# Performance work log

Measured on AMD Instinct MI355X. Metric: run time of the kernel, lower is better.

The kernel has to match this reference:

```python
import jax, jax.numpy as jnp
import numpy as np

MODES_KEPT = 64  # n_modes=(128,) -> 128//2 rfft modes retained (neuralop convention)
N_LAYERS = 4     # neuralop FNO default n_layers
PAD_FRAC = 0.1   # domain_padding


def setup_inputs() -> dict:
    key = jax.random.key(0)
    ks = jax.random.split(key, 24)
    B, T, P = 128, 4096, 64
    E, Hemb, W = 32, 128, 64
    Cin = 4 + E            # 36
    Hl = 2 * W             # lifting hidden (lifting_channel_ratio=2)
    Hp = 2 * W             # projection hidden

    def w(k, sh):
        fan_in = sh[0]
        return jax.random.normal(k, sh, jnp.float32) * (fan_in ** -0.5)

    spec_scale = 1.0 / (W * W)
    return {
        "v_terminals": jax.random.normal(ks[0], (B, 4, T), jnp.float32),
        "physical_params": jax.random.normal(ks[1], (B, P), jnp.float32),
        # DeviceEmbedding MLP: P -> Hemb -> Hemb -> E
        "emb_w1": w(ks[2], (P, Hemb)), "emb_b1": jnp.zeros((Hemb,), jnp.float32),
        "emb_w2": w(ks[3], (Hemb, Hemb)), "emb_b2": jnp.zeros((Hemb,), jnp.float32),
        "emb_w3": w(ks[4], (Hemb, E)), "emb_b3": jnp.zeros((E,), jnp.float32),
        # FNO lifting channel-MLP: Cin -> Hl -> W (pointwise over time)
        "lift_w1": w(ks[5], (Cin, Hl)), "lift_b1": jnp.zeros((Hl,), jnp.float32),
        "lift_w2": w(ks[6], (Hl, W)), "lift_b2": jnp.zeros((W,), jnp.float32),
        # spectral conv complex weights, stored as real/imag: (L, Cin=W, Cout=W, M)
        "spec_wr": jax.random.normal(ks[7], (N_LAYERS, W, W, MODES_KEPT), jnp.float32) * spec_scale,
        "spec_wi": jax.random.normal(ks[8], (N_LAYERS, W, W, MODES_KEPT), jnp.float32) * spec_scale,
        # linear (1x1) skips per layer
        "skip_w": jax.random.normal(ks[9], (N_LAYERS, W, W), jnp.float32) * (W ** -0.5),
        "skip_b": jnp.zeros((N_LAYERS, W), jnp.float32),
        # projection channel-MLP: W -> Hp -> 1
        "proj_w1": w(ks[10], (W, Hp)), "proj_b1": jnp.zeros((Hp,), jnp.float32),
        "proj_w2": w(ks[11], (Hp, 1)), "proj_b2": jnp.zeros((1,), jnp.float32),
    }


def _chan_mlp(x, w, b):
    # pointwise channel linear on (B, C, T)
    return jnp.einsum("bct,cd->bdt", x, w) + b[None, :, None]


def reference(v_terminals, physical_params,
              emb_w1, emb_b1, emb_w2, emb_b2, emb_w3, emb_b3,
              lift_w1, lift_b1, lift_w2, lift_b2,
              spec_wr, spec_wi, skip_w, skip_b,
              proj_w1, proj_b1, proj_w2, proj_b2):
    silu = jax.nn.silu
    gelu = jax.nn.gelu
    B, _, T = v_terminals.shape
    # device embedding: Linear-GELU-Linear-GELU-Linear-Tanh
    h = gelu(physical_params @ emb_w1 + emb_b1)
    h = gelu(h @ emb_w2 + emb_b2)
    h = jnp.tanh(h @ emb_w3 + emb_b3)                       # (B, E)
    lat = jnp.broadcast_to(h[:, :, None], (B, h.shape[1], T))
    x = jnp.concatenate([v_terminals, lat], axis=1)          # (B, 36, T)
    # lifting
    x = _chan_mlp(silu(_chan_mlp(x, lift_w1, lift_b1) * 0 + _chan_mlp(x, lift_w1, lift_b1)), lift_w2, lift_b2) if False else None
    x = jnp.concatenate([v_terminals, lat], axis=1)
    x = _chan_mlp(x, lift_w1, lift_b1)
    x = silu(x)
    x = _chan_mlp(x, lift_w2, lift_b2)                       # (B, W, T)
    pad = int(round(PAD_FRAC * T))
    x = jnp.pad(x, ((0, 0), (0, 0), (0, pad)))
    Tp = T + pad
    nfreq = Tp // 2 + 1
    for l in range(N_LAYERS):
        hpre = silu(x)                                       # preactivation
        skip = jnp.einsum("bct,oc->bot", hpre, skip_w[l]) + skip_b[l][None, :, None]
        xf = jnp.fft.rfft(hpre, axis=-1)                     # (B, W, nfreq) complex
        wc = spec_wr[l] + 1j * spec_wi[l]                    # (W, W, M)
        yf = jnp.einsum("bcm,com->bom", xf[..., :MODES_KEPT], wc)
        out_ft = jnp.pad(yf, ((0, 0), (0, 0), (0, nfreq - MODES_KEPT)))
        x = jnp.fft.irfft(out_ft, n=Tp, axis=-1) + skip
    x = x[..., :T]                                           # unpad
    # projection
    x = _chan_mlp(x, proj_w1, proj_b1)
    x = silu(x)
    x = _chan_mlp(x, proj_w2, proj_b2)                       # (B, 1, T)
    return x
```

## Files before the change

kernel.cpp:

```cpp
#include <hip/hip_runtime.h>
#include <math.h>

#define B_     128
#define T_     4096
#define TP_    4506
#define TPAD_  4608
#define KSPLIT 6
#define NL_    4

typedef __attribute__((ext_vector_type(8))) short bf16x8;
typedef __attribute__((ext_vector_type(4))) float f32x4;
typedef unsigned short u16;

__device__ __forceinline__ float silu_f(float x){
  return x / (1.0f + expf(-x));
}
__device__ __forceinline__ float gelu_f(float x){
  float u = x + 0.044715f*x*x*x;
  return 0.5f*x*(1.0f + tanhf(0.7978845608028654f*u));
}
__device__ __forceinline__ u16 bf16_rne(float f){
  unsigned u = __float_as_uint(f);
  unsigned r = u + 0x7FFFu + ((u >> 16) & 1u);
  return (u16)(r >> 16);
}
__device__ __forceinline__ void bf16_split(float f, u16& h, u16& l){
  h = bf16_rne(f);
  float fh = __uint_as_float(((unsigned)h) << 16);
  l = bf16_rne(f - fh);
}
__device__ __forceinline__ void silu_split(float v, u16& h, u16& l){
  float s = v / (1.0f + __expf(-v));
  bf16_split(s, h, l);
}
__device__ __forceinline__ f32x4 mfma16(bf16x8 a, bf16x8 b, f32x4 c){
  return __builtin_amdgcn_mfma_f32_16x16x32_bf16(a, b, c, 0, 0, 0);
}

#define FMA8x8(ACC, A0, A1, B0, B1) do {                                   \
  float av_[8] = {A0.x,A0.y,A0.z,A0.w,A1.x,A1.y,A1.z,A1.w};                \
  float bv_[8] = {B0.x,B0.y,B0.z,B0.w,B1.x,B1.y,B1.z,B1.w};                \
  _Pragma("unroll")                                                        \
  for(int i_=0;i_<8;i_++){                                                 \
    _Pragma("unroll")                                                      \
    for(int j_=0;j_<8;j_++) ACC[i_][j_] += av_[i_]*bv_[j_];                \
  }                                                                        \
} while(0)

__global__ __launch_bounds__(256) void k_tables(u16* __restrict__ fwdFh,
    u16* __restrict__ fwdFl, u16* __restrict__ invFh, u16* __restrict__ invFl){
  int idx = blockIdx.x*256 + threadIdx.x;
  if(idx >= TPAD_*64) return;
  int t = idx >> 6, m = idx & 63;
  float c = 0.f, s = 0.f;
  if(t < TP_){
    int r = (int)(((long long)m * (long long)t) % TP_);
    double ang = 6.283185307179586476925287 * (double)r / (double)TP_;
    c = (float)cos(ang);
    s = -(float)sin(ang);
  }
  u16 ch, cl, sh, sl;
  bf16_split(c, ch, cl);
  bf16_split(s, sh, sl);
  fwdFh[t*128 + m] = ch;      fwdFl[t*128 + m] = cl;
  fwdFh[t*128 + 64 + m] = sh; fwdFl[t*128 + 64 + m] = sl;
  invFh[(long)m*TPAD_ + t] = ch;      invFl[(long)m*TPAD_ + t] = cl;
  invFh[(long)(64+m)*TPAD_ + t] = sh; invFl[(long)(64+m)*TPAD_ + t] = sl;
}

__global__ __launch_bounds__(256) void k_prep(const float* __restrict__ skw,
    u16* __restrict__ skwh, u16* __restrict__ skwl){
  int i = blockIdx.x*256 + threadIdx.x;
  if(i >= NL_*64*64) return;
  u16 h, l; bf16_split(skw[i], h, l);
  skwh[i] = h; skwl[i] = l;
}

__global__ __launch_bounds__(128) void k_embed(
    const float* __restrict__ pp,
    const float* __restrict__ ew1, const float* __restrict__ eb1,
    const float* __restrict__ ew2, const float* __restrict__ eb2,
    const float* __restrict__ ew3, const float* __restrict__ eb3,
    const float* __restrict__ lw1, const float* __restrict__ lb1,
    float* __restrict__ latb)
{
  int b = blockIdx.x, tid = threadIdx.x;
  __shared__ float p[64], h1[128], h2[128], e[32];
  if(tid < 64) p[tid] = pp[b*64 + tid];
  __syncthreads();
  {
    float z = eb1[tid];
    for(int j=0;j<64;j++) z += p[j]*ew1[j*128 + tid];
    h1[tid] = gelu_f(z);
  }
  __syncthreads();
  {
    float z = eb2[tid];
    for(int j=0;j<128;j++) z += h1[j]*ew2[j*128 + tid];
    h2[tid] = gelu_f(z);
  }
  __syncthreads();
  if(tid < 32){
    float z = eb3[tid];
    for(int j=0;j<128;j++) z += h2[j]*ew3[j*32 + tid];
    e[tid] = tanhf(z);
  }
  __syncthreads();
  {
    float v = lb1[tid];
    for(int c=0;c<32;c++) v += e[c]*lw1[(4+c)*128 + tid];
    latb[b*128 + tid] = v;
  }
}

__global__ __launch_bounds__(128) void k_lift(
    const float* __restrict__ vterm, const float* __restrict__ latb,
    const float* __restrict__ lw1,  const float* __restrict__ lw2,
    const float* __restrict__ lb2,  float* __restrict__ x)
{
  int tt = blockIdx.x, b = blockIdx.y, tid = threadIdx.x;
  int t0 = tt*128;
  if(t0 >= T_){
    int r = tid >> 1, tcb = (tid & 1)*64;
    float4 z4 = make_float4(0.f,0.f,0.f,0.f);
    #pragma unroll
    for(int q=0;q<16;q++)
      *(float4*)(x + ((long)b*64 + r)*TPAD_ + t0 + tcb + q*4) = z4;
    return;
  }
  __shared__ float w2s[128*64];
  __shared__ float zt[64*132];
  __shared__ float vt[4*128];
  #pragma unroll
  for(int q=0;q<16;q++){
    int idx = q*512 + tid*4;
    *(float4*)(w2s + idx) = *(const float4*)(lw2 + idx);
  }
  {
    int c = tid >> 5, tc = (tid & 31)*4;
    *(float4*)(vt + c*128 + tc) =
      *(const float4*)(vterm + ((long)b*4 + c)*T_ + t0 + tc);
  }
  int tx = tid & 15, ty = tid >> 4;
  float acc[8][8];
  #pragma unroll
  for(int i=0;i<8;i++){
    #pragma unroll
    for(int j=0;j<8;j++) acc[i][j] = 0.f;
  }
  for(int ch=0; ch<2; ++ch){
    __syncthreads();
    {
      int dl = tid >> 1, d = ch*64 + dl, tcb = (tid & 1)*64;
      float lb  = latb[b*128 + d];
      float wc0 = lw1[0*128 + d], wc1 = lw1[1*128 + d];
      float wc2 = lw1[2*128 + d], wc3 = lw1[3*128 + d];
      #pragma unroll
      for(int q=0;q<16;q++){
        int tc = tcb + q*4;
        float4 v0 = *(const float4*)(vt + 0*128 + tc);
        float4 v1 = *(const float4*)(vt + 1*128 + tc);
        float4 v2 = *(const float4*)(vt + 2*128 + tc);
        float4 v3 = *(const float4*)(vt + 3*128 + tc);
        float4 z;
        z.x = silu_f(lb + wc0*v0.x + wc1*v1.x + wc2*v2.x + wc3*v3.x);
        z.y = silu_f(lb + wc0*v0.y + wc1*v1.y + wc2*v2.y + wc3*v3.y);
        z.z = silu_f(lb + wc0*v0.z + wc1*v1.z + wc2*v2.z + wc3*v3.z);
        z.w = silu_f(lb + wc0*v0.w + wc1*v1.w + wc2*v2.w + wc3*v3.w);
        *(float4*)(zt + dl*132 + tc) = z;
      }
    }
    __syncthreads();
    #pragma unroll 4
    for(int k=0;k<64;k++){
      int d = ch*64 + k;
      float4 a0 = *(const float4*)(w2s + d*64 + 8*ty);
      float4 a1 = *(const float4*)(w2s + d*64 + 8*ty + 4);
      float4 b0 = *(const float4*)(zt + k*132 + 8*tx);
      float4 b1 = *(const float4*)(zt + k*132 + 8*tx + 4);
      FMA8x8(acc, a0, a1, b0, b1);
    }
  }
  #pragma unroll
  for(int i=0;i<8;i++){
    int w = 8*ty + i;
    float bias = lb2[w];
    float* dst = x + ((long)b*64 + w)*TPAD_ + t0 + 8*tx;
    *(float4*)(dst)   = make_float4(acc[i][0]+bias, acc[i][1]+bias, acc[i][2]+bias, acc[i][3]+bias);
    *(float4*)(dst+4) = make_float4(acc[i][4]+bias, acc[i][5]+bias, acc[i][6]+bias, acc[i][7]+bias);
  }
}

__global__ __launch_bounds__(256) void k_dft_mfma(
    const float* __restrict__ x, const u16* __restrict__ invFh,
    const u16* __restrict__ invFl, float* __restrict__ xfp)
{
  int b = blockIdx.x, s = blockIdx.y;
  int tid = threadIdx.x;
  int lane = tid & 63, w = tid >> 6;
  int l15 = lane & 15, lhi = lane >> 4;
  int n0 = w*32;
  __shared__ u16 ah[64*128];
  __shared__ u16 al[64*128];
  f32x4 acc[4][2];
  #pragma unroll
  for(int mi=0;mi<4;mi++){
    #pragma unroll
    for(int ni=0;ni<2;ni++) acc[mi][ni] = (f32x4){0.f,0.f,0.f,0.f};
  }
  for(int ch=0; ch<6; ++ch){
    int k0 = s*768 + ch*128;
    __syncthreads();
    {
      int c = tid >> 2;
      const float* xr = x + ((long)b*64 + c)*TPAD_ + k0;
      int swz = (c & 7) << 4;
      #pragma unroll
      for(int q=0;q<8;q++){
        int tl = ((tid & 3) + 4*q)*4;
        float4 v = *(const float4*)(xr + tl);
        ushort4 hv, lv;
        silu_split(v.x, hv.x, lv.x);
        silu_split(v.y, hv.y, lv.y);
        silu_split(v.z, hv.z, lv.z);
        silu_split(v.w, hv.w, lv.w);
        int byt = (c*256 + tl*2) ^ swz;
        *(ushort4*)((char*)ah + byt) = hv;
        *(ushort4*)((char*)al + byt) = lv;
      }
    }
    __syncthreads();
    #pragma unroll
    for(int ks=0; ks<4; ++ks){
      bf16x8 Ah[4], Al[4], Bh[2], Bl[2];
      #pragma unroll
      for(int mi=0;mi<4;mi++){
        int c = mi*16 + l15;
        int byt = (c*256 + (ks*32 + lhi*8)*2) ^ ((c & 7) << 4);
        Ah[mi] = *(bf16x8*)((char*)ah + byt);
        Al[mi] = *(bf16x8*)((char*)al + byt);
      }
      #pragma unroll
      for(int ni=0;ni<2;ni++){
        int j = n0 + ni*16 + l15;
        long off = (long)j*TPAD_ + k0 + ks*32 + lhi*8;
        Bh[ni] = *(const bf16x8*)(invFh + off);
        Bl[ni] = *(const bf16x8*)(invFl + off);
      }
      #pragma unroll
      for(int mi=0;mi<4;mi++){
        #pragma unroll
        for(int ni=0;ni<2;ni++){
          acc[mi][ni] = mfma16(Ah[mi], Bh[ni], acc[mi][ni]);
          acc[mi][ni] = mfma16(Al[mi], Bh[ni], acc[mi][ni]);
          acc[mi][ni] = mfma16(Ah[mi], Bl[ni], acc[mi][ni]);
        }
      }
    }
  }
  #pragma unroll
  for(int mi=0;mi<4;mi++){
    #pragma unroll
    for(int ni=0;ni<2;ni++){
      #pragma unroll
      for(int r=0;r<4;r++){
        int row = mi*16 + lhi*4 + r;
        int j = n0 + ni*16 + l15;
        xfp[((long)s*8192 + b*64 + row)*128 + j] = acc[mi][ni][r];
      }
    }
  }
}

__global__ __launch_bounds__(512) void k_spectral(
    const float* __restrict__ xfp, const float* __restrict__ wr_,
    const float* __restrict__ wi_, u16* __restrict__ coefh,
    u16* __restrict__ coefl, int l)
{
  int b = blockIdx.x, mh = blockIdx.y, tid = threadIdx.x;
  const float* wr = wr_ + (long)l*262144;
  const float* wi = wi_ + (long)l*262144;
  __shared__ float xr[64*36], xi[64*36];
  {
    int c = tid >> 3, mm0 = (tid & 7)*4;
    long base = ((long)(b*64 + c))*128 + mh*32 + mm0;
    float4 sr = make_float4(0.f,0.f,0.f,0.f), si = sr;
    #pragma unroll
    for(int s2=0;s2<KSPLIT;s2++){
      const float* p = xfp + (long)s2*1048576 + base;
      float4 a = *(const float4*)(p);
      float4 d = *(const float4*)(p + 64);
      sr.x += a.x; sr.y += a.y; sr.z += a.z; sr.w += a.w;
      si.x += d.x; si.y += d.y; si.z += d.z; si.w += d.w;
    }
    *(float4*)(xr + c*36 + mm0) = sr;
    *(float4*)(xi + c*36 + mm0) = si;
  }
  __syncthreads();
  int tx = tid & 15, ty = tid >> 4;
  float ar[2][2] = {{0.f,0.f},{0.f,0.f}};
  float ai[2][2] = {{0.f,0.f},{0.f,0.f}};
  #pragma unroll 2
  for(int c=0;c<64;c++){
    float x0r = xr[c*36 + 2*tx], x1r = xr[c*36 + 2*tx + 1];
    float x0i = xi[c*36 + 2*tx], x1i = xi[c*36 + 2*tx + 1];
    #pragma unroll
    for(int oi=0;oi<2;oi++){
      int o = 2*ty + oi;
      long wofs = ((long)(c*64 + o))*64 + mh*32 + 2*tx;
      float2 wrv = *(const float2*)(wr + wofs);
      float2 wiv = *(const float2*)(wi + wofs);
      ar[oi][0] += x0r*wrv.x - x0i*wiv.x;
      ai[oi][0] += x0r*wiv.x + x0i*wrv.x;
      ar[oi][1] += x1r*wrv.y - x1i*wiv.y;
      ai[oi][1] += x1r*wiv.y + x1i*wrv.y;
    }
  }
  #pragma unroll
  for(int j=0;j<2;j++){
    int m = mh*32 + 2*tx + j;
    float sc = (m==0) ? (1.0f/(float)TP_) : (2.0f/(float)TP_);
    #pragma unroll
    for(int oi=0;oi<2;oi++){
      int o = 2*ty + oi;
      long base = ((long)b*64 + o)*128;
      u16 h, l2;
      bf16_split(sc*ar[oi][j], h, l2);
      coefh[base + m] = h; coefl[base + m] = l2;
      bf16_split(sc*ai[oi][j], h, l2);
      coefh[base + 64 + m] = h; coefl[base + 64 + m] = l2;
    }
  }
}

__global__ __launch_bounds__(256) void k_idft_mfma(
    float* __restrict__ x, const u16* __restrict__ coefh,
    const u16* __restrict__ coefl, const u16* __restrict__ fwdFh,
    const u16* __restrict__ fwdFl, const u16* __restrict__ skwh,
    const u16* __restrict__ skwl, const float* __restrict__ sb_, int lay)
{
  int tt = blockIdx.x, b = blockIdx.y, tid = threadIdx.x;
  int t0 = tt*128;
  int lane = tid & 63, w = tid >> 6;
  int l15 = lane & 15, lhi = lane >> 4;
  int n0 = w*32;
  __shared__ u16 hh[128*64];
  __shared__ u16 hl[128*64];
  {
    int cp = tid & 31, tg = tid >> 3 >> 2;
    int c0 = cp*2;
    const float* xr0 = x + ((long)b*64 + c0)*TPAD_ + t0 + tg*16;
    const float* xr1 = xr0 + TPAD_;
    #pragma unroll
    for(int q=0;q<4;q++){
      float4 v0 = *(const float4*)(xr0 + q*4);
      float4 v1 = *(const float4*)(xr1 + q*4);
      float e0[4] = {v0.x, v0.y, v0.z, v0.w};
      float e1[4] = {v1.x, v1.y, v1.z, v1.w};
      #pragma unroll
      for(int i=0;i<4;i++){
        int t = tg*16 + q*4 + i;
        u16 h0, l0, h1, l1;
        silu_split(e0[i], h0, l0);
        silu_split(e1[i], h1, l1);
        int byt = (t*128 + c0*2) ^ ((t & 7) << 4);
        *(ushort2*)((char*)hh + byt) = make_ushort2(h0, h1);
        *(ushort2*)((char*)hl + byt) = make_ushort2(l0, l1);
      }
    }
  }
  f32x4 acc[4][2];
  #pragma unroll
  for(int mi=0;mi<4;mi++){
    #pragma unroll
    for(int ni=0;ni<2;ni++) acc[mi][ni] = (f32x4){0.f,0.f,0.f,0.f};
  }
  #pragma unroll
  for(int ks=0; ks<4; ++ks){
    bf16x8 Ah[4], Al[4], Bh[2], Bl[2];
    #pragma unroll
    for(int mi=0;mi<4;mi++){
      int o = mi*16 + l15;
      long off = ((long)(b*64 + o))*128 + ks*32 + lhi*8;
      Ah[mi] = *(const bf16x8*)(coefh + off);
      Al[mi] = *(const bf16x8*)(coefl + off);
    }
    #pragma unroll
    for(int ni=0;ni<2;ni++){
      int t = t0 + n0 + ni*16 + l15;
      long off = (long)t*128 + ks*32 + lhi*8;
      Bh[ni] = *(const bf16x8*)(fwdFh + off);
      Bl[ni] = *(const bf16x8*)(fwdFl + off);
    }
    #pragma unroll
    for(int mi=0;mi<4;mi++){
      #pragma unroll
      for(int ni=0;ni<2;ni++){
        acc[mi][ni] = mfma16(Ah[mi], Bh[ni], acc[mi][ni]);
        acc[mi][ni] = mfma16(Al[mi], Bh[ni], acc[mi][ni]);
        acc[mi][ni] = mfma16(Ah[mi], Bl[ni], acc[mi][ni]);
      }
    }
  }
  __syncthreads();
  #pragma unroll
  for(int ks=0; ks<2; ++ks){
    bf16x8 Ah[4], Al[4], Bh[2], Bl[2];
    #pragma unroll
    for(int mi=0;mi<4;mi++){
      int o = mi*16 + l15;
      long off = (long)lay*4096 + o*64 + ks*32 + lhi*8;
      Ah[mi] = *(const bf16x8*)(skwh + off);
      Al[mi] = *(const bf16x8*)(skwl + off);
    }
    #pragma unroll
    for(int ni=0;ni<2;ni++){
      int t = n0 + ni*16 + l15;
      int byt = (t*128 + (ks*32 + lhi*8)*2) ^ ((t & 7) << 4);
      Bh[ni] = *(bf16x8*)((char*)hh + byt);
      Bl[ni] = *(bf16x8*)((char*)hl + byt);
    }
    #pragma unroll
    for(int mi=0;mi<4;mi++){
      #pragma unroll
      for(int ni=0;ni<2;ni++){
        acc[mi][ni] = mfma16(Ah[mi], Bh[ni], acc[mi][ni]);
        acc[mi][ni] = mfma16(Al[mi], Bh[ni], acc[mi][ni]);
        acc[mi][ni] = mfma16(Ah[mi], Bl[ni], acc[mi][ni]);
      }
    }
  }
  #pragma unroll
  for(int mi=0;mi<4;mi++){
    #pragma unroll
    for(int ni=0;ni<2;ni++){
      #pragma unroll
      for(int r=0;r<4;r++){
        int o = mi*16 + lhi*4 + r;
        int t = t0 + n0 + ni*16 + l15;
        float v = acc[mi][ni][r] + sb_[lay*64 + o];
        if(t >= TP_) v = 0.f;
        x[((long)b*64 + o)*TPAD_ + t] = v;
      }
    }
  }
}

__global__ __launch_bounds__(256) void k_proj(
    const float* __restrict__ x,  const float* __restrict__ pw1,
    const float* __restrict__ pb1, const float* __restrict__ pw2,
    const float* __restrict__ pb2, float* __restrict__ out)
{
  int tt = blockIdx.x, b = blockIdx.y, tid = threadIdx.x;
  int t0 = tt*128;
  __shared__ float w1s[64*128];
  __shared__ float xt[64*132];
  __shared__ float red[16*132];
  #pragma unroll
  for(int q=0;q<8;q++){
    int idx = q*1024 + tid*4;
    *(float4*)(w1s + idx) = *(const float4*)(pw1 + idx);
  }
  {
    int w = tid >> 2, tc0 = (tid & 3)*4;
    #pragma unroll
    for(int q=0;q<8;q++){
      int tc = tc0 + q*16;
      *(float4*)(xt + w*132 + tc) =
        *(const float4*)(x + ((long)b*64 + w)*TPAD_ + t0 + tc);
    }
  }
  __syncthreads();
  int tx = tid & 15, ty = tid >> 4;
  float acc[8][8];
  #pragma unroll
  for(int i=0;i<8;i++){
    #pragma unroll
    for(int j=0;j<8;j++) acc[i][j] = 0.f;
  }
  #pragma unroll 4
  for(int k=0;k<64;k++){
    float4 a0 = *(const float4*)(w1s + k*128 + 8*ty);
    float4 a1 = *(const float4*)(w1s + k*128 + 8*ty + 4);
    float4 b0 = *(const float4*)(xt + k*132 + 8*tx);
    float4 b1 = *(const float4*)(xt + k*132 + 8*tx + 4);
    FMA8x8(acc, a0, a1, b0, b1);
  }
  float part[8];
  #pragma unroll
  for(int j=0;j<8;j++) part[j] = 0.f;
  #pragma unroll
  for(int i=0;i<8;i++){
    int d = 8*ty + i;
    float bb = pb1[d], w2v = pw2[d];
    #pragma unroll
    for(int j=0;j<8;j++) part[j] += w2v * silu_f(acc[i][j] + bb);
  }
  *(float4*)(red + ty*132 + 8*tx)     = make_float4(part[0],part[1],part[2],part[3]);
  *(float4*)(red + ty*132 + 8*tx + 4) = make_float4(part[4],part[5],part[6],part[7]);
  __syncthreads();
  if(tid < 128){
    float ssum = pb2[0];
    #pragma unroll
    for(int y=0;y<16;y++) ssum += red[y*132 + tid];
    out[(long)b*T_ + t0 + tid] = ssum;
  }
}

extern "C" void kernel_launch(void* const* d_in, const int* in_sizes, int n_in,
                              void* d_out, int out_size, void* d_ws, size_t ws_size,
                              hipStream_t stream)
{
  const float* vterm = (const float*)d_in[0];
  const float* pp    = (const float*)d_in[1];
  const float* ew1   = (const float*)d_in[2];
  const float* eb1   = (const float*)d_in[3];
  const float* ew2   = (const float*)d_in[4];
  const float* eb2   = (const float*)d_in[5];
  const float* ew3   = (const float*)d_in[6];
  const float* eb3   = (const float*)d_in[7];
  const float* lw1   = (const float*)d_in[8];
  const float* lb1   = (const float*)d_in[9];
  const float* lw2   = (const float*)d_in[10];
  const float* lb2   = (const float*)d_in[11];
  const float* swr   = (const float*)d_in[12];
  const float* swi   = (const float*)d_in[13];
  const float* skw   = (const float*)d_in[14];
  const float* skb   = (const float*)d_in[15];
  const float* pw1   = (const float*)d_in[16];
  const float* pb1   = (const float*)d_in[17];
  const float* pw2   = (const float*)d_in[18];
  const float* pb2   = (const float*)d_in[19];
  float* out = (float*)d_out;
  float* ws  = (float*)d_ws;

  float* x    = ws;
  float* xfp  = x + (long)B_*64*TPAD_;
  u16* coefh  = (u16*)(xfp + (long)KSPLIT*8192*128);
  u16* coefl  = coefh + 1048576;
  u16* fwdFh  = coefl + 1048576;
  u16* fwdFl  = fwdFh + 589824;
  u16* invFh  = fwdFl + 589824;
  u16* invFl  = invFh + 589824;
  u16* skwh   = invFl + 589824;
  u16* skwl   = skwh + 16384;
  float* latb = (float*)coefh;

  k_tables<<<(TPAD_*64 + 255)/256, 256, 0, stream>>>(fwdFh, fwdFl, invFh, invFl);
  k_prep<<<(NL_*64*64 + 255)/256, 256, 0, stream>>>(skw, skwh, skwl);
  k_embed<<<B_, 128, 0, stream>>>(pp, ew1, eb1, ew2, eb2, ew3, eb3, lw1, lb1, latb);
  k_lift<<<dim3(TPAD_/128, B_), 128, 0, stream>>>(vterm, latb, lw1, lw2, lb2, x);
  for(int l=0;l<NL_;l++){
    k_dft_mfma<<<dim3(B_, KSPLIT), 256, 0, stream>>>(x, invFh, invFl, xfp);
    k_spectral<<<dim3(B_, 2), 512, 0, stream>>>(xfp, swr, swi, coefh, coefl, l);
    k_idft_mfma<<<dim3(TPAD_/128, B_), 256, 0, stream>>>(
        x, coefh, coefl, fwdFh, fwdFl, skwh, skwl, skb, l);
  }
  k_proj<<<dim3(T_/128, B_), 256, 0, stream>>>(x, pw1, pb1, pw2, pb2, out);
}
```

Measured before the change: 1.379 ms.

## Store SiLU-activated state as split bf16 and move lift GEMM to MFMA

The activation state between layers is now kept as precomputed SiLU(x) in split hi/lo bf16 form rather than fp32 x. The SiLU and bf16 split are applied once in the producer epilogue (lift and idft) instead of being recomputed in both the DFT and IDFT consumers. The lift's second channel-MLP moves from scalar FMA to 3-pass bf16 MFMA using a pre-transposed, split weight. The DFT kernel now streams split operands directly from global memory without LDS staging. Epilogues go through LDS for coalesced stores, which adds synchronisation and changes the rounding path slightly.

```diff
diff --git a/kernel.cpp b/kernel.cpp
--- a/kernel.cpp
+++ b/kernel.cpp
@@ -32,6 +32,9 @@
 __device__ __forceinline__ void silu_split(float v, u16& h, u16& l){
   float s = v / (1.0f + __expf(-v));
   bf16_split(s, h, l);
+}
+__device__ __forceinline__ float bf2f(u16 h){
+  return __uint_as_float(((unsigned)h) << 16);
 }
 __device__ __forceinline__ f32x4 mfma16(bf16x8 a, bf16x8 b, f32x4 c){
   return __builtin_amdgcn_mfma_f32_16x16x32_bf16(a, b, c, 0, 0, 0);
@@ -69,11 +72,19 @@
 }
 
 __global__ __launch_bounds__(256) void k_prep(const float* __restrict__ skw,
-    u16* __restrict__ skwh, u16* __restrict__ skwl){
+    u16* __restrict__ skwh, u16* __restrict__ skwl,
+    const float* __restrict__ lw2, u16* __restrict__ lw2Th,
+    u16* __restrict__ lw2Tl){
   int i = blockIdx.x*256 + threadIdx.x;
-  if(i >= NL_*64*64) return;
-  u16 h, l; bf16_split(skw[i], h, l);
-  skwh[i] = h; skwl[i] = l;
+  if(i < NL_*64*64){
+    u16 h, l; bf16_split(skw[i], h, l);
+    skwh[i] = h; skwl[i] = l;
+  } else if(i < NL_*64*64 + 64*128){
+    int j = i - NL_*64*64;
+    int w = j >> 7, d = j & 127;
+    u16 h, l; bf16_split(lw2[d*64 + w], h, l);
+    lw2Th[j] = h; lw2Tl[j] = l;
+  }
 }
 
 __global__ __launch_bounds__(128) void k_embed(
@@ -113,161 +124,172 @@
   }
 }
 
-__global__ __launch_bounds__(128) void k_lift(
+__global__ __launch_bounds__(256) void k_lift(
     const float* __restrict__ vterm, const float* __restrict__ latb,
-    const float* __restrict__ lw1,  const float* __restrict__ lw2,
-    const float* __restrict__ lb2,  float* __restrict__ x)
+    const float* __restrict__ lw1,  const u16* __restrict__ lw2Th,
+    const u16* __restrict__ lw2Tl, const float* __restrict__ lb2,
+    u16* __restrict__ hx, u16* __restrict__ lx)
 {
   int tt = blockIdx.x, b = blockIdx.y, tid = threadIdx.x;
   int t0 = tt*128;
   if(t0 >= T_){
-    int r = tid >> 1, tcb = (tid & 1)*64;
-    float4 z4 = make_float4(0.f,0.f,0.f,0.f);
-    #pragma unroll
-    for(int q=0;q<16;q++)
-      *(float4*)(x + ((long)b*64 + r)*TPAD_ + t0 + tcb + q*4) = z4;
+    int r = tid >> 2, t00 = (tid & 3)*32;
+    bf16x8 z8 = (bf16x8){0,0,0,0,0,0,0,0};
+    long base = ((long)b*64 + r)*TPAD_ + t0 + t00;
+    #pragma unroll
+    for(int q=0;q<4;q++){
+      *(bf16x8*)(hx + base + q*8) = z8;
+      *(bf16x8*)(lx + base + q*8) = z8;
+    }
     return;
   }
-  __shared__ float w2s[128*64];
-  __shared__ float zt[64*132];
-  __shared__ float vt[4*128];
-  #pragma unroll
-  for(int q=0;q<16;q++){
-    int idx = q*512 + tid*4;
-    *(float4*)(w2s + idx) = *(const float4*)(lw2 + idx);
-  }
-  {
+  __shared__ u16 zz[32768];
+  u16* zh = zz;
+  u16* zl = zz + 16384;
+  __shared__ float vt[512], lw1c[512], latbs[128];
+  if(tid < 128){
     int c = tid >> 5, tc = (tid & 31)*4;
     *(float4*)(vt + c*128 + tc) =
       *(const float4*)(vterm + ((long)b*4 + c)*T_ + t0 + tc);
-  }
-  int tx = tid & 15, ty = tid >> 4;
-  float acc[8][8];
-  #pragma unroll
-  for(int i=0;i<8;i++){
-    #pragma unroll
-    for(int j=0;j<8;j++) acc[i][j] = 0.f;
-  }
-  for(int ch=0; ch<2; ++ch){
-    __syncthreads();
-    {
-      int dl = tid >> 1, d = ch*64 + dl, tcb = (tid & 1)*64;
-      float lb  = latb[b*128 + d];
-      float wc0 = lw1[0*128 + d], wc1 = lw1[1*128 + d];
-      float wc2 = lw1[2*128 + d], wc3 = lw1[3*128 + d];
-      #pragma unroll
-      for(int q=0;q<16;q++){
-        int tc = tcb + q*4;
-        float4 v0 = *(const float4*)(vt + 0*128 + tc);
-        float4 v1 = *(const float4*)(vt + 1*128 + tc);
-        float4 v2 = *(const float4*)(vt + 2*128 + tc);
-        float4 v3 = *(const float4*)(vt + 3*128 + tc);
-        float4 z;
-        z.x = silu_f(lb + wc0*v0.x + wc1*v1.x + wc2*v2.x + wc3*v3.x);
-        z.y = silu_f(lb + wc0*v0.y + wc1*v1.y + wc2*v2.y + wc3*v3.y);
-        z.z = silu_f(lb + wc0*v0.z + wc1*v1.z + wc2*v2.z + wc3*v3.z);
-        z.w = silu_f(lb + wc0*v0.w + wc1*v1.w + wc2*v2.w + wc3*v3.w);
-        *(float4*)(zt + dl*132 + tc) = z;
-      }
-    }
-    __syncthreads();
-    #pragma unroll 4
-    for(int k=0;k<64;k++){
-      int d = ch*64 + k;
-      float4 a0 = *(const float4*)(w2s + d*64 + 8*ty);
-      float4 a1 = *(const float4*)(w2s + d*64 + 8*ty + 4);
-      float4 b0 = *(const float4*)(zt + k*132 + 8*tx);
-      float4 b1 = *(const float4*)(zt + k*132 + 8*tx + 4);
-      FMA8x8(acc, a0, a1, b0, b1);
-    }
-  }
-  #pragma unroll
-  for(int i=0;i<8;i++){
-    int w = 8*ty + i;
-    float bias = lb2[w];
-    float* dst = x + ((long)b*64 + w)*TPAD_ + t0 + 8*tx;
-    *(float4*)(dst)   = make_float4(acc[i][0]+bias, acc[i][1]+bias, acc[i][2]+bias, acc[i][3]+bias);
-    *(float4*)(dst+4) = make_float4(acc[i][4]+bias, acc[i][5]+bias, acc[i][6]+bias, acc[i][7]+bias);
-  }
-}
-
-__global__ __launch_bounds__(256) void k_dft_mfma(
-    const float* __restrict__ x, const u16* __restrict__ invFh,
-    const u16* __restrict__ invFl, float* __restrict__ xfp)
-{
-  int b = blockIdx.x, s = blockIdx.y;
-  int tid = threadIdx.x;
+  } else {
+    int i = (tid - 128)*4;
+    *(float4*)(lw1c + i) = *(const float4*)(lw1 + i);
+  }
+  if(tid < 32)
+    *(float4*)(latbs + tid*4) = *(const float4*)(latb + b*128 + tid*4);
+  __syncthreads();
+  {
+    int t = tid >> 1, dh = (tid & 1)*64;
+    float v0 = vt[t], v1 = vt[128+t], v2 = vt[256+t], v3 = vt[384+t];
+    int swz = (t & 7) << 4;
+    #pragma unroll
+    for(int q=0;q<16;q++){
+      int d0 = dh + q*4;
+      float4 w0 = *(const float4*)(lw1c + d0);
+      float4 w1 = *(const float4*)(lw1c + 128 + d0);
+      float4 w2 = *(const float4*)(lw1c + 256 + d0);
+      float4 w3 = *(const float4*)(lw1c + 384 + d0);
+      float4 lb = *(const float4*)(latbs + d0);
+      u16 h0,h1,h2,h3,l0,l1,l2,l3;
+      silu_split(lb.x + w0.x*v0 + w1.x*v1 + w2.x*v2 + w3.x*v3, h0, l0);
+      silu_split(lb.y + w0.y*v0 + w1.y*v1 + w2.y*v2 + w3.y*v3, h1, l1);
+      silu_split(lb.z + w0.z*v0 + w1.z*v1 + w2.z*v2 + w3.z*v3, h2, l2);
+      silu_split(lb.w + w0.w*v0 + w1.w*v1 + w2.w*v2 + w3.w*v3, h3, l3);
+      int byt = (t*256 + d0*2) ^ swz;
+      uint2 hv = make_uint2((unsigned)h0 | ((unsigned)h1<<16),
+                            (unsigned)h2 | ((unsigned)h3<<16));
+      uint2 lv = make_uint2((unsigned)l0 | ((unsigned)l1<<16),
+                            (unsigned)l2 | ((unsigned)l3<<16));
+      *(uint2*)((char*)zh + byt) = hv;
+      *(uint2*)((char*)zl + byt) = lv;
+    }
+  }
+  __syncthreads();
   int lane = tid & 63, w = tid >> 6;
   int l15 = lane & 15, lhi = lane >> 4;
   int n0 = w*32;
-  __shared__ u16 ah[64*128];
-  __shared__ u16 al[64*128];
   f32x4 acc[4][2];
   #pragma unroll
   for(int mi=0;mi<4;mi++){
     #pragma unroll
     for(int ni=0;ni<2;ni++) acc[mi][ni] = (f32x4){0.f,0.f,0.f,0.f};
   }
-  for(int ch=0; ch<6; ++ch){
-    int k0 = s*768 + ch*128;
-    __syncthreads();
-    {
-      int c = tid >> 2;
-      const float* xr = x + ((long)b*64 + c)*TPAD_ + k0;
-      int swz = (c & 7) << 4;
-      #pragma unroll
-      for(int q=0;q<8;q++){
-        int tl = ((tid & 3) + 4*q)*4;
-        float4 v = *(const float4*)(xr + tl);
-        ushort4 hv, lv;
-        silu_split(v.x, hv.x, lv.x);
-        silu_split(v.y, hv.y, lv.y);
-        silu_split(v.z, hv.z, lv.z);
-        silu_split(v.w, hv.w, lv.w);
-        int byt = (c*256 + tl*2) ^ swz;
-        *(ushort4*)((char*)ah + byt) = hv;
-        *(ushort4*)((char*)al + byt) = lv;
-      }
-    }
-    __syncthreads();
-    #pragma unroll
-    for(int ks=0; ks<4; ++ks){
-      bf16x8 Ah[4], Al[4], Bh[2], Bl[2];
-      #pragma unroll
-      for(int mi=0;mi<4;mi++){
-        int c = mi*16 + l15;
-        int byt = (c*256 + (ks*32 + lhi*8)*2) ^ ((c & 7) << 4);
-        Ah[mi] = *(bf16x8*)((char*)ah + byt);
-        Al[mi] = *(bf16x8*)((char*)al + byt);
-      }
+  #pragma unroll
+  for(int ks=0; ks<4; ++ks){
+    bf16x8 Ah[4], Al[4], Bh[2], Bl[2];
+    #pragma unroll
+    for(int mi=0;mi<4;mi++){
+      int o = mi*16 + l15;
+      long off = (long)o*128 + ks*32 + lhi*8;
+      Ah[mi] = *(const bf16x8*)(lw2Th + off);
+      Al[mi] = *(const bf16x8*)(lw2Tl + off);
+    }
+    #pragma unroll
+    for(int ni=0;ni<2;ni++){
+      int t = n0 + ni*16 + l15;
+      int byt = (t*256 + (ks*32 + lhi*8)*2) ^ ((t & 7) << 4);
+      Bh[ni] = *(bf16x8*)((char*)zh + byt);
+      Bl[ni] = *(bf16x8*)((char*)zl + byt);
+    }
+    #pragma unroll
+    for(int mi=0;mi<4;mi++){
       #pragma unroll
       for(int ni=0;ni<2;ni++){
-        int j = n0 + ni*16 + l15;
-        long off = (long)j*TPAD_ + k0 + ks*32 + lhi*8;
-        Bh[ni] = *(const bf16x8*)(invFh + off);
-        Bl[ni] = *(const bf16x8*)(invFl + off);
+        acc[mi][ni] = mfma16(Ah[mi], Bh[ni], acc[mi][ni]);
+        acc[mi][ni] = mfma16(Al[mi], Bh[ni], acc[mi][ni]);
+        acc[mi][ni] = mfma16(Ah[mi], Bl[ni], acc[mi][ni]);
       }
-      #pragma unroll
-      for(int mi=0;mi<4;mi++){
-        #pragma unroll
-        for(int ni=0;ni<2;ni++){
-          acc[mi][ni] = mfma16(Ah[mi], Bh[ni], acc[mi][ni]);
-          acc[mi][ni] = mfma16(Al[mi], Bh[ni], acc[mi][ni]);
-          acc[mi][ni] = mfma16(Ah[mi], Bl[ni], acc[mi][ni]);
-        }
-      }
-    }
-  }
+    }
+  }
+  __syncthreads();
+  float* fo = (float*)zz;
   #pragma unroll
   for(int mi=0;mi<4;mi++){
     #pragma unroll
     for(int ni=0;ni<2;ni++){
       #pragma unroll
       for(int r=0;r<4;r++){
-        int row = mi*16 + lhi*4 + r;
-        int j = n0 + ni*16 + l15;
-        xfp[((long)s*8192 + b*64 + row)*128 + j] = acc[mi][ni][r];
+        int o = mi*16 + lhi*4 + r;
+        int tl = n0 + ni*16 + l15;
+        fo[o*128 + (tl ^ ((o&7)<<2))] = acc[mi][ni][r];
       }
+    }
+  }
+  __syncthreads();
+  #pragma unroll
+  for(int q=0;q<8;q++){
+    int idx = q*256 + tid;
+    int o = idx >> 5, tb = idx & 31;
+    float4 rd = *(const float4*)(fo + o*128 + ((tb*4) ^ ((o&7)<<2)));
+    float bias = lb2[o];
+    u16 h0,h1,h2,h3,l0,l1,l2,l3;
+    silu_split(rd.x + bias, h0, l0);
+    silu_split(rd.y + bias, h1, l1);
+    silu_split(rd.z + bias, h2, l2);
+    silu_split(rd.w + bias, h3, l3);
+    long base = ((long)b*64 + o)*TPAD_ + t0 + tb*4;
+    *(uint2*)(hx + base) = make_uint2((unsigned)h0 | ((unsigned)h1<<16),
+                                      (unsigned)h2 | ((unsigned)h3<<16));
+    *(uint2*)(lx + base) = make_uint2((unsigned)l0 | ((unsigned)l1<<16),
+                                      (unsigned)l2 | ((unsigned)l3<<16));
+  }
+}
+
+__global__ __launch_bounds__(256) void k_dft(
+    const u16* __restrict__ hx, const u16* __restrict__ lx,
+    const u16* __restrict__ invFh, const u16* __restrict__ invFl,
+    float* __restrict__ xfp)
+{
+  int b = blockIdx.x, s = blockIdx.y, tid = threadIdx.x;
+  int lane = tid & 63, w = tid >> 6;
+  int l15 = lane & 15, lhi = lane >> 4;
+  long k0 = (long)s*768;
+  const u16* rowAh = hx + ((long)b*64 + w*16 + l15)*TPAD_ + k0 + lhi*8;
+  const u16* rowAl = lx + ((long)b*64 + w*16 + l15)*TPAD_ + k0 + lhi*8;
+  const u16* rowBh = invFh + (long)l15*TPAD_ + k0 + lhi*8;
+  const u16* rowBl = invFl + (long)l15*TPAD_ + k0 + lhi*8;
+  f32x4 acc[8];
+  #pragma unroll
+  for(int ni=0;ni<8;ni++) acc[ni] = (f32x4){0.f,0.f,0.f,0.f};
+  #pragma unroll 2
+  for(int ks=0; ks<24; ++ks){
+    bf16x8 Ah = *(const bf16x8*)(rowAh + ks*32);
+    bf16x8 Al = *(const bf16x8*)(rowAl + ks*32);
+    #pragma unroll
+    for(int ni=0;ni<8;ni++){
+      bf16x8 Bh = *(const bf16x8*)(rowBh + (long)ni*16*TPAD_ + ks*32);
+      bf16x8 Bl = *(const bf16x8*)(rowBl + (long)ni*16*TPAD_ + ks*32);
+      acc[ni] = mfma16(Ah, Bh, acc[ni]);
+      acc[ni] = mfma16(Al, Bh, acc[ni]);
+      acc[ni] = mfma16(Ah, Bl, acc[ni]);
+    }
+  }
+  #pragma unroll
+  for(int ni=0;ni<8;ni++){
+    #pragma unroll
+    for(int r=0;r<4;r++){
+      int row = w*16 + lhi*4 + r;
+      xfp[((long)s*8192 + b*64 + row)*128 + ni*16 + l15] = acc[ni][r];
     }
   }
 }
@@ -333,40 +355,48 @@
   }
 }
 
-__global__ __launch_bounds__(256) void k_idft_mfma(
-    float* __restrict__ x, const u16* __restrict__ coefh,
-    const u16* __restrict__ coefl, const u16* __restrict__ fwdFh,
-    const u16* __restrict__ fwdFl, const u16* __restrict__ skwh,
-    const u16* __restrict__ skwl, const float* __restrict__ sb_, int lay)
+__global__ __launch_bounds__(256) void k_idft(
+    u16* __restrict__ hx, u16* __restrict__ lx,
+    const u16* __restrict__ coefh, const u16* __restrict__ coefl,
+    const u16* __restrict__ fwdFh, const u16* __restrict__ fwdFl,
+    const u16* __restrict__ skwh, const u16* __restrict__ skwl,
+    const float* __restrict__ sb_, int lay, int last)
 {
   int tt = blockIdx.x, b = blockIdx.y, tid = threadIdx.x;
   int t0 = tt*128;
   int lane = tid & 63, w = tid >> 6;
   int l15 = lane & 15, lhi = lane >> 4;
   int n0 = w*32;
-  __shared__ u16 hh[128*64];
-  __shared__ u16 hl[128*64];
+  __shared__ u16 sh_[16384];
+  u16* hh = sh_;
+  u16* hl = sh_ + 8192;
   {
-    int cp = tid & 31, tg = tid >> 3 >> 2;
-    int c0 = cp*2;
-    const float* xr0 = x + ((long)b*64 + c0)*TPAD_ + t0 + tg*16;
-    const float* xr1 = xr0 + TPAD_;
-    #pragma unroll
-    for(int q=0;q<4;q++){
-      float4 v0 = *(const float4*)(xr0 + q*4);
-      float4 v1 = *(const float4*)(xr1 + q*4);
-      float e0[4] = {v0.x, v0.y, v0.z, v0.w};
-      float e1[4] = {v1.x, v1.y, v1.z, v1.w};
-      #pragma unroll
-      for(int i=0;i<4;i++){
-        int t = tg*16 + q*4 + i;
-        u16 h0, l0, h1, l1;
-        silu_split(e0[i], h0, l0);
-        silu_split(e1[i], h1, l1);
-        int byt = (t*128 + c0*2) ^ ((t & 7) << 4);
-        *(ushort2*)((char*)hh + byt) = make_ushort2(h0, h1);
-        *(ushort2*)((char*)hl + byt) = make_ushort2(l0, l1);
-      }
+    int c0 = (tid & 31)*2, tg = tid >> 5;
+    const u16* ph0 = hx + ((long)b*64 + c0)*TPAD_ + t0 + tg*16;
+    const u16* ph1 = ph0 + TPAD_;
+    const u16* pl0 = lx + ((long)b*64 + c0)*TPAD_ + t0 + tg*16;
+    const u16* pl1 = pl0 + TPAD_;
+    bf16x8 h0a = *(const bf16x8*)(ph0),     h0b = *(const bf16x8*)(ph0 + 8);
+    bf16x8 h1a = *(const bf16x8*)(ph1),     h1b = *(const bf16x8*)(ph1 + 8);
+    bf16x8 l0a = *(const bf16x8*)(pl0),     l0b = *(const bf16x8*)(pl0 + 8);
+    bf16x8 l1a = *(const bf16x8*)(pl1),     l1b = *(const bf16x8*)(pl1 + 8);
+    #pragma unroll
+    for(int i=0;i<8;i++){
+      int t = tg*16 + i;
+      int byt = (t*128 + c0*2) ^ ((t & 7) << 4);
+      *(unsigned*)((char*)hh + byt) =
+        (unsigned)(u16)h0a[i] | ((unsigned)(u16)h1a[i] << 16);
+      *(unsigned*)((char*)hl + byt) =
+        (unsigned)(u16)l0a[i] | ((unsigned)(u16)l1a[i] << 16);
+    }
+    #pragma unroll
+    for(int i=0;i<8;i++){
+      int t = tg*16 + 8 + i;
+      int byt = (t*128 + c0*2) ^ ((t & 7) << 4);
+      *(unsigned*)((char*)hh + byt) =
+        (unsigned)(u16)h0b[i] | ((unsigned)(u16)h1b[i] << 16);
+      *(unsigned*)((char*)hl + byt) =
+        (unsigned)(u16)l0b[i] | ((unsigned)(u16)l1b[i] << 16);
     }
   }
   f32x4 acc[4][2];
@@ -430,6 +460,8 @@
       }
     }
   }
+  __syncthreads();
+  float* fo = (float*)sh_;
   #pragma unroll
   for(int mi=0;mi<4;mi++){
     #pragma unroll
@@ -437,19 +469,43 @@
       #pragma unroll
       for(int r=0;r<4;r++){
         int o = mi*16 + lhi*4 + r;
-        int t = t0 + n0 + ni*16 + l15;
-        float v = acc[mi][ni][r] + sb_[lay*64 + o];
-        if(t >= TP_) v = 0.f;
-        x[((long)b*64 + o)*TPAD_ + t] = v;
+        int tl = n0 + ni*16 + l15;
+        fo[o*128 + (tl ^ ((o&7)<<2))] = acc[mi][ni][r];
       }
     }
   }
+  __syncthreads();
+  #pragma unroll
+  for(int q=0;q<8;q++){
+    int idx = q*256 + tid;
+    int o = idx >> 5, tb = idx & 31;
+    float4 rd = *(const float4*)(fo + o*128 + ((tb*4) ^ ((o&7)<<2)));
+    float bias = sb_[lay*64 + o];
+    float v[4] = {rd.x + bias, rd.y + bias, rd.z + bias, rd.w + bias};
+    int tg = t0 + tb*4;
+    #pragma unroll
+    for(int j=0;j<4;j++){
+      if(tg + j >= TP_) v[j] = 0.f;
+      else if(!last)    v[j] = silu_f(v[j]);
+    }
+    u16 h0,h1,h2,h3,l0,l1,l2,l3;
+    bf16_split(v[0], h0, l0);
+    bf16_split(v[1], h1, l1);
+    bf16_split(v[2], h2, l2);
+    bf16_split(v[3], h3, l3);
+    long base = ((long)b*64 + o)*TPAD_ + t0 + tb*4;
+    *(uint2*)(hx + base) = make_uint2((unsigned)h0 | ((unsigned)h1<<16),
+                                      (unsigned)h2 | ((unsigned)h3<<16));
+    *(uint2*)(lx + base) = make_uint2((unsigned)l0 | ((unsigned)l1<<16),
+                                      (unsigned)l2 | ((unsigned)l3<<16));
+  }
 }
 
 __global__ __launch_bounds__(256) void k_proj(
-    const float* __restrict__ x,  const float* __restrict__ pw1,
-    const float* __restrict__ pb1, const float* __restrict__ pw2,
-    const float* __restrict__ pb2, float* __restrict__ out)
+    const u16* __restrict__ hx, const u16* __restrict__ lx,
+    const float* __restrict__ pw1, const float* __restrict__ pb1,
+    const float* __restrict__ pw2, const float* __restrict__ pb2,
+    float* __restrict__ out)
 {
   int tt = blockIdx.x, b = blockIdx.y, tid = threadIdx.x;
   int t0 = tt*128;
@@ -462,12 +518,20 @@
     *(float4*)(w1s + idx) = *(const float4*)(pw1 + idx);
   }
   {
-    int w = tid >> 2, tc0 = (tid & 3)*4;
-    #pragma unroll
-    for(int q=0;q<8;q++){
-      int tc = tc0 + q*16;
-      *(float4*)(xt + w*132 + tc) =
-        *(const float4*)(x + ((long)b*64 + w)*TPAD_ + t0 + tc);
+    int w = tid >> 2, tq = tid & 3;
+    const u16* hrow = hx + ((long)b*64 + w)*TPAD_ + t0;
+    const u16* lrow = lx + ((long)b*64 + w)*TPAD_ + t0;
+    #pragma unroll
+    for(int q=0;q<4;q++){
+      int tl = (tq + q*4)*8;
+      bf16x8 hv = *(const bf16x8*)(hrow + tl);
+      bf16x8 lv = *(const bf16x8*)(lrow + tl);
+      float f[8];
+      #pragma unroll
+      for(int i=0;i<8;i++)
+        f[i] = bf2f((u16)hv[i]) + bf2f((u16)lv[i]);
+      *(float4*)(xt + w*132 + tl)     = make_float4(f[0],f[1],f[2],f[3]);
+      *(float4*)(xt + w*132 + tl + 4) = make_float4(f[4],f[5],f[6],f[7]);
     }
   }
   __syncthreads();
@@ -532,11 +596,11 @@
   const float* pw2   = (const float*)d_in[18];
   const float* pb2   = (const float*)d_in[19];
   float* out = (float*)d_out;
-  float* ws  = (float*)d_ws;
-
-  float* x    = ws;
-  float* xfp  = x + (long)B_*64*TPAD_;
-  u16* coefh  = (u16*)(xfp + (long)KSPLIT*8192*128);
+
+  u16* hx     = (u16*)d_ws;
+  u16* lxp    = hx + 37748736;
+  float* xfp  = (float*)(lxp + 37748736);
+  u16* coefh  = (u16*)(xfp + 6291456);
   u16* coefl  = coefh + 1048576;
   u16* fwdFh  = coefl + 1048576;
   u16* fwdFl  = fwdFh + 589824;
@@ -545,16 +609,20 @@
   u16* skwh   = invFl + 589824;
   u16* skwl   = skwh + 16384;
   float* latb = (float*)coefh;
+  u16* lw2Th  = coefl;
+  u16* lw2Tl  = coefl + 8192;
 
   k_tables<<<(TPAD_*64 + 255)/256, 256, 0, stream>>>(fwdFh, fwdFl, invFh, invFl);
-  k_prep<<<(NL_*64*64 + 255)/256, 256, 0, stream>>>(skw, skwh, skwl);
+  k_prep<<<(NL_*64*64 + 64*128 + 255)/256, 256, 0, stream>>>(
+      skw, skwh, skwl, lw2, lw2Th, lw2Tl);
   k_embed<<<B_, 128, 0, stream>>>(pp, ew1, eb1, ew2, eb2, ew3, eb3, lw1, lb1, latb);
-  k_lift<<<dim3(TPAD_/128, B_), 128, 0, stream>>>(vterm, latb, lw1, lw2, lb2, x);
+  k_lift<<<dim3(TPAD_/128, B_), 256, 0, stream>>>(
+      vterm, latb, lw1, lw2Th, lw2Tl, lb2, hx, lxp);
   for(int l=0;l<NL_;l++){
-    k_dft_mfma<<<dim3(B_, KSPLIT), 256, 0, stream>>>(x, invFh, invFl, xfp);
+    k_dft<<<dim3(B_, KSPLIT), 256, 0, stream>>>(hx, lxp, invFh, invFl, xfp);
     k_spectral<<<dim3(B_, 2), 512, 0, stream>>>(xfp, swr, swi, coefh, coefl, l);
-    k_idft_mfma<<<dim3(TPAD_/128, B_), 256, 0, stream>>>(
-        x, coefh, coefl, fwdFh, fwdFl, skwh, skwl, skb, l);
-  }
-  k_proj<<<dim3(T_/128, B_), 256, 0, stream>>>(x, pw1, pb1, pw2, pb2, out);
-}
+    k_idft<<<dim3(TPAD_/128, B_), 256, 0, stream>>>(
+        hx, lxp, coefh, coefl, fwdFh, fwdFl, skwh, skwl, skb, l, (l==NL_-1) ? 1 : 0);
+  }
+  k_proj<<<dim3(T_/128, B_), 256, 0, stream>>>(hx, lxp, pw1, pb1, pw2, pb2, out);
+}
```

After: 1.660 ms. +20.4%, slower.
